# Optimization experiments

Measured on AMD Instinct MI355X. Metric: run time of the kernel, lower is better.

The kernel has to match this reference:

```python
import jax, jax.numpy as jnp
import numpy as np


def _causal_conv(x, w, b, dilation):
    # x: (B, Cin, N), w: (Cout, Cin, K) -> causal: left-pad (K-1)*dilation
    pad = (w.shape[-1] - 1) * dilation
    y = jax.lax.conv_general_dilated(
        x, w, window_strides=(1,), padding=[(pad, 0)],
        rhs_dilation=(dilation,), dimension_numbers=('NCH', 'OIH', 'NCH'))
    return y + b[None, :, None]


def setup_inputs() -> dict:
    key = jax.random.key(0)
    ks = jax.random.split(key, 8)
    B, N, C, L = 8, 32768, 16, 30
    s = 0.1  # weight scale to avoid gate saturation
    return {
        'x': jax.random.normal(ks[0], (B, N), dtype=jnp.float32) * 1000.0,  # int16-like samples
        'lengths': jax.random.randint(ks[1], (B,), N // 2, N),
        'w0': jax.random.normal(ks[2], (C, 1, 2), dtype=jnp.float32) * s,
        'b0': jnp.zeros((C,), jnp.float32),
        'wf': jax.random.normal(ks[3], (L - 1, C, C, 2), dtype=jnp.float32) * s,
        'bf': jnp.zeros((L - 1, C), jnp.float32),
        'wg': jax.random.normal(ks[4], (L - 1, C, C, 2), dtype=jnp.float32) * s,
        'bg': jnp.zeros((L - 1, C), jnp.float32),
        'wa': jax.random.normal(ks[5], (64, C), dtype=jnp.float32) * s,
        'ba': jnp.zeros((64,), jnp.float32),
        'wo': jax.random.normal(ks[6], (256, 64), dtype=jnp.float32) * s,
        'bo': jnp.zeros((256,), jnp.float32),
    }


def reference(x, lengths, w0, b0, wf, bf, wg, bg, wa, ba, wo, bo):
    L = wf.shape[0] + 1  # total layers (layer 0 is plain causal conv)
    xin = (x / 32768.0)[:, None, :]            # (B,1,N), int16 normalization 65536/2
    out0 = _causal_conv(xin, w0, b0, 1)        # (B,C,N)
    agg = out0                                 # skip aggregate
    h = xin + out0                             # residual input (broadcast 1->C channels)
    for i in range(1, L):                      # fixed small layer count
        d = 2 ** (i % 10)
        f = _causal_conv(h, wf[i - 1], bf[i - 1], d)
        g = _causal_conv(h, wg[i - 1], bg[i - 1], d)
        out = jnp.tanh(f) * jax.nn.sigmoid(g)  # gated activation unit
        agg = agg + out
        h = h + out
    a = jnp.einsum('oc,bcn->bon', wa, jax.nn.relu(agg)) + ba[None, :, None]  # agregate1x1
    o = jnp.einsum('oc,bcn->bon', wo, jax.nn.relu(a)) + bo[None, :, None]    # output1x1
    o = jax.nn.log_softmax(o, axis=1)
    mask = (jnp.arange(o.shape[-1]) < lengths[:, None]).astype(o.dtype)      # (B,N)
    return o * mask[:, None, :]
```

## Files before the change

kernel.cpp:

```cpp
#include <hip/hip_runtime.h>

#define NSEQ 32768
#define NB 8
#define NC 16
#define LBLK 1024
#define LPX (LBLK / 8)

__device__ __forceinline__ float sigm_f(float x) {
    return __fdividef(1.f, 1.f + __expf(-x));
}
__device__ __forceinline__ float tanh_f(float x) {
    return __fdividef(2.f, 1.f + __expf(-2.f * x)) - 1.f;
}

__device__ __forceinline__ int swz_bid() {
    int bid = blockIdx.x;
    return (bid & 7) * LPX + (bid >> 3);
}

__global__ __launch_bounds__(256) void k_layer0(
    const float* __restrict__ x, const float* __restrict__ w0,
    const float* __restrict__ b0, float* __restrict__ h)
{
    int tid = swz_bid() * 256 + threadIdx.x;
    int n = tid & (NSEQ - 1);
    const float inv = 1.f / 32768.f;
    float xc = x[tid] * inv;
    float xp = (n >= 1) ? x[tid - 1] * inv : 0.f;
    float v[NC];
#pragma unroll
    for (int c = 0; c < NC; c++) {
        float o = w0[c * 2] * xp + w0[c * 2 + 1] * xc + b0[c];
        v[c] = xc + o;
    }
    float4* ph = (float4*)(h + (size_t)tid * NC);
#pragma unroll
    for (int i = 0; i < 4; i++)
        ph[i] = make_float4(v[i * 4], v[i * 4 + 1], v[i * 4 + 2], v[i * 4 + 3]);
}

__global__ __launch_bounds__(256) void k_layer(
    const float* __restrict__ hin, float* __restrict__ hout,
    const float* __restrict__ wf, const float* __restrict__ bf,
    const float* __restrict__ wg, const float* __restrict__ bg, int d)
{
    int tid = swz_bid() * 256 + threadIdx.x;
    int n = tid & (NSEQ - 1);

    float hc[NC], hp[NC];
    {
        const float4* pc = (const float4*)(hin + (size_t)tid * NC);
#pragma unroll
        for (int i = 0; i < 4; i++) {
            float4 t = pc[i];
            hc[i * 4] = t.x; hc[i * 4 + 1] = t.y; hc[i * 4 + 2] = t.z; hc[i * 4 + 3] = t.w;
        }
    }
    if (n >= d) {
        const float4* pp = (const float4*)(hin + (size_t)(tid - d) * NC);
#pragma unroll
        for (int i = 0; i < 4; i++) {
            float4 t = pp[i];
            hp[i * 4] = t.x; hp[i * 4 + 1] = t.y; hp[i * 4 + 2] = t.z; hp[i * 4 + 3] = t.w;
        }
    } else {
#pragma unroll
        for (int i = 0; i < NC; i++) hp[i] = 0.f;
    }

    float f[NC], g[NC];
#pragma unroll
    for (int co = 0; co < NC; co++) { f[co] = bf[co]; g[co] = bg[co]; }

#pragma unroll
    for (int ci = 0; ci < NC; ci++) {
        float xp = hp[ci], xc = hc[ci];
#pragma unroll
        for (int co = 0; co < NC; co++) {
            f[co] = fmaf(wf[(co * NC + ci) * 2 + 0], xp, f[co]);
            f[co] = fmaf(wf[(co * NC + ci) * 2 + 1], xc, f[co]);
            g[co] = fmaf(wg[(co * NC + ci) * 2 + 0], xp, g[co]);
            g[co] = fmaf(wg[(co * NC + ci) * 2 + 1], xc, g[co]);
        }
    }

    float v[NC];
#pragma unroll
    for (int co = 0; co < NC; co++) {
        float outv = tanh_f(f[co]) * sigm_f(g[co]);
        v[co] = hc[co] + outv;
    }
    float4* po = (float4*)(hout + (size_t)tid * NC);
#pragma unroll
    for (int i = 0; i < 4; i++)
        po[i] = make_float4(v[i * 4], v[i * 4 + 1], v[i * 4 + 2], v[i * 4 + 3]);
}

__global__ __launch_bounds__(512, 2) void k_final(
    const float* __restrict__ hfin, const float* __restrict__ x,
    const int* __restrict__ lengths,
    const float* __restrict__ wa, const float* __restrict__ ba,
    const float* __restrict__ wo, const float* __restrict__ bo,
    float* __restrict__ out)
{
    __shared__ float s_r[64][17];
    __shared__ float s_ra[64][65];
    __shared__ float s_red[2][8][64];

    int t = threadIdx.x;
    int p = t & 63;
    int q = __builtin_amdgcn_readfirstlane(t >> 6);
    int blk = blockIdx.x;
    int b = blk >> 9;
    int n0 = (blk & 511) << 6;
    int n = n0 + p;
    size_t pos = (size_t)b * NSEQ + n;
    float xin = x[pos] * (1.f / 32768.f);

    if (q < 4) {
        const float4* ph = (const float4*)(hfin + pos * NC);
        float4 v = ph[q];
        s_r[p][q * 4 + 0] = fmaxf(v.x - xin, 0.f);
        s_r[p][q * 4 + 1] = fmaxf(v.y - xin, 0.f);
        s_r[p][q * 4 + 2] = fmaxf(v.z - xin, 0.f);
        s_r[p][q * 4 + 3] = fmaxf(v.w - xin, 0.f);
    }
    __syncthreads();

    {
        float r[NC];
#pragma unroll
        for (int c = 0; c < NC; c++) r[c] = s_r[p][c];
#pragma unroll
        for (int jj = 0; jj < 8; jj++) {
            int j = q * 8 + jj;
            float acc = ba[j];
#pragma unroll
            for (int c = 0; c < NC; c++) acc = fmaf(wa[j * NC + c], r[c], acc);
            s_ra[p][j] = fmaxf(acc, 0.f);
        }
    }
    __syncthreads();

    float ra[64];
#pragma unroll
    for (int j = 0; j < 64; j++) ra[j] = s_ra[p][j];

    float o[32];
    float m = -1e30f;
#pragma unroll 4
    for (int kk = 0; kk < 32; kk++) {
        int k = q * 32 + kk;
        float acc = bo[k];
#pragma unroll
        for (int j = 0; j < 64; j++) acc = fmaf(wo[k * 64 + j], ra[j], acc);
        o[kk] = acc;
        m = fmaxf(m, acc);
    }
    s_red[0][q][p] = m;
    __syncthreads();
    m = fmaxf(fmaxf(fmaxf(s_red[0][0][p], s_red[0][1][p]),
                    fmaxf(s_red[0][2][p], s_red[0][3][p])),
              fmaxf(fmaxf(s_red[0][4][p], s_red[0][5][p]),
                    fmaxf(s_red[0][6][p], s_red[0][7][p])));
    float s = 0.f;
#pragma unroll
    for (int kk = 0; kk < 32; kk++) s += __expf(o[kk] - m);
    s_red[1][q][p] = s;
    __syncthreads();
    s = ((s_red[1][0][p] + s_red[1][1][p]) + (s_red[1][2][p] + s_red[1][3][p]))
      + ((s_red[1][4][p] + s_red[1][5][p]) + (s_red[1][6][p] + s_red[1][7][p]));
    float lse = m + __logf(s);

    bool valid = n < lengths[b];
    float* po = out + ((size_t)b * 256 + q * 32) * NSEQ + n;
#pragma unroll
    for (int kk = 0; kk < 32; kk++) {
        float v = valid ? (o[kk] - lse) : 0.f;
        __builtin_nontemporal_store(v, &po[(size_t)kk * NSEQ]);
    }
}

extern "C" void kernel_launch(void* const* d_in, const int* in_sizes, int n_in,
                              void* d_out, int out_size, void* d_ws, size_t ws_size,
                              hipStream_t stream) {
    const float* x   = (const float*)d_in[0];
    const int* lens  = (const int*)d_in[1];
    const float* w0  = (const float*)d_in[2];
    const float* b0  = (const float*)d_in[3];
    const float* wf  = (const float*)d_in[4];
    const float* bf  = (const float*)d_in[5];
    const float* wg  = (const float*)d_in[6];
    const float* bg  = (const float*)d_in[7];
    const float* wa  = (const float*)d_in[8];
    const float* ba  = (const float*)d_in[9];
    const float* wo  = (const float*)d_in[10];
    const float* bo  = (const float*)d_in[11];
    float* out = (float*)d_out;

    float* hA = (float*)d_ws;
    float* hB = hA + (size_t)NB * NSEQ * NC;

    const int total = NB * NSEQ;
    dim3 blk(256);
    dim3 grd(total / 256);

    k_layer0<<<grd, blk, 0, stream>>>(x, w0, b0, hA);

    float* cur = hA;
    float* nxt = hB;
    for (int i = 1; i <= 29; i++) {
        int d = 1 << (i % 10);
        k_layer<<<grd, blk, 0, stream>>>(cur, nxt,
                                         wf + (size_t)(i - 1) * NC * NC * 2,
                                         bf + (size_t)(i - 1) * NC,
                                         wg + (size_t)(i - 1) * NC * NC * 2,
                                         bg + (size_t)(i - 1) * NC, d);
        float* tmp = cur; cur = nxt; nxt = tmp;
    }

    dim3 fgrd(NB * (NSEQ / 64));
    k_final<<<fgrd, dim3(512), 0, stream>>>(cur, x, lens, wa, ba, wo, bo, out);
}
```

Measured before the change: 670.0 us.

## Split layer kernel output channels across four waves per position

```diff
diff --git a/kernel.cpp b/kernel.cpp
--- a/kernel.cpp
+++ b/kernel.cpp
@@ -5,24 +5,22 @@
 #define NC 16
 #define LBLK 1024
 #define LPX (LBLK / 8)
+#define QGRD 4096
+#define QPX (QGRD / 8)
 
 __device__ __forceinline__ float sigm_f(float x) {
     return __fdividef(1.f, 1.f + __expf(-x));
 }
 __device__ __forceinline__ float tanh_f(float x) {
     return __fdividef(2.f, 1.f + __expf(-2.f * x)) - 1.f;
-}
-
-__device__ __forceinline__ int swz_bid() {
-    int bid = blockIdx.x;
-    return (bid & 7) * LPX + (bid >> 3);
 }
 
 __global__ __launch_bounds__(256) void k_layer0(
     const float* __restrict__ x, const float* __restrict__ w0,
     const float* __restrict__ b0, float* __restrict__ h)
 {
-    int tid = swz_bid() * 256 + threadIdx.x;
+    int bid = blockIdx.x;
+    int tid = ((bid & 7) * LPX + (bid >> 3)) * 256 + threadIdx.x;
     int n = tid & (NSEQ - 1);
     const float inv = 1.f / 32768.f;
     float xc = x[tid] * inv;
@@ -44,56 +42,60 @@
     const float* __restrict__ wf, const float* __restrict__ bf,
     const float* __restrict__ wg, const float* __restrict__ bg, int d)
 {
-    int tid = swz_bid() * 256 + threadIdx.x;
-    int n = tid & (NSEQ - 1);
+    int bid = blockIdx.x;
+    int lbid = (bid & 7) * QPX + (bid >> 3);
+    int t = threadIdx.x;
+    int pos = lbid * 64 + (t & 63);
+    int q = __builtin_amdgcn_readfirstlane(t >> 6);
+    int n = pos & (NSEQ - 1);
 
     float hc[NC], hp[NC];
     {
-        const float4* pc = (const float4*)(hin + (size_t)tid * NC);
+        const float4* pc = (const float4*)(hin + (size_t)pos * NC);
 #pragma unroll
         for (int i = 0; i < 4; i++) {
-            float4 t = pc[i];
-            hc[i * 4] = t.x; hc[i * 4 + 1] = t.y; hc[i * 4 + 2] = t.z; hc[i * 4 + 3] = t.w;
+            float4 tv = pc[i];
+            hc[i * 4] = tv.x; hc[i * 4 + 1] = tv.y; hc[i * 4 + 2] = tv.z; hc[i * 4 + 3] = tv.w;
         }
     }
     if (n >= d) {
-        const float4* pp = (const float4*)(hin + (size_t)(tid - d) * NC);
+        const float4* pp = (const float4*)(hin + (size_t)(pos - d) * NC);
 #pragma unroll
         for (int i = 0; i < 4; i++) {
-            float4 t = pp[i];
-            hp[i * 4] = t.x; hp[i * 4 + 1] = t.y; hp[i * 4 + 2] = t.z; hp[i * 4 + 3] = t.w;
+            float4 tv = pp[i];
+            hp[i * 4] = tv.x; hp[i * 4 + 1] = tv.y; hp[i * 4 + 2] = tv.z; hp[i * 4 + 3] = tv.w;
         }
     } else {
 #pragma unroll
         for (int i = 0; i < NC; i++) hp[i] = 0.f;
     }
 
-    float f[NC], g[NC];
-#pragma unroll
-    for (int co = 0; co < NC; co++) { f[co] = bf[co]; g[co] = bg[co]; }
+    const int c0 = q * 4;
+    float f[4], g[4];
+#pragma unroll
+    for (int j = 0; j < 4; j++) { f[j] = bf[c0 + j]; g[j] = bg[c0 + j]; }
 
 #pragma unroll
     for (int ci = 0; ci < NC; ci++) {
         float xp = hp[ci], xc = hc[ci];
 #pragma unroll
-        for (int co = 0; co < NC; co++) {
-            f[co] = fmaf(wf[(co * NC + ci) * 2 + 0], xp, f[co]);
-            f[co] = fmaf(wf[(co * NC + ci) * 2 + 1], xc, f[co]);
-            g[co] = fmaf(wg[(co * NC + ci) * 2 + 0], xp, g[co]);
-            g[co] = fmaf(wg[(co * NC + ci) * 2 + 1], xc, g[co]);
-        }
-    }
-
-    float v[NC];
-#pragma unroll
-    for (int co = 0; co < NC; co++) {
-        float outv = tanh_f(f[co]) * sigm_f(g[co]);
-        v[co] = hc[co] + outv;
-    }
-    float4* po = (float4*)(hout + (size_t)tid * NC);
-#pragma unroll
-    for (int i = 0; i < 4; i++)
-        po[i] = make_float4(v[i * 4], v[i * 4 + 1], v[i * 4 + 2], v[i * 4 + 3]);
+        for (int j = 0; j < 4; j++) {
+            int co = c0 + j;
+            f[j] = fmaf(wf[(co * NC + ci) * 2 + 0], xp, f[j]);
+            f[j] = fmaf(wf[(co * NC + ci) * 2 + 1], xc, f[j]);
+            g[j] = fmaf(wg[(co * NC + ci) * 2 + 0], xp, g[j]);
+            g[j] = fmaf(wg[(co * NC + ci) * 2 + 1], xc, g[j]);
+        }
+    }
+
+    float v[4];
+#pragma unroll
+    for (int j = 0; j < 4; j++) {
+        float outv = tanh_f(f[j]) * sigm_f(g[j]);
+        v[j] = hc[c0 + j] + outv;
+    }
+    float4* po = (float4*)(hout + (size_t)pos * NC + c0);
+    po[0] = make_float4(v[0], v[1], v[2], v[3]);
 }
 
 __global__ __launch_bounds__(512, 2) void k_final(
@@ -201,17 +203,13 @@
     float* hA = (float*)d_ws;
     float* hB = hA + (size_t)NB * NSEQ * NC;
 
-    const int total = NB * NSEQ;
-    dim3 blk(256);
-    dim3 grd(total / 256);
-
-    k_layer0<<<grd, blk, 0, stream>>>(x, w0, b0, hA);
+    k_layer0<<<dim3(LBLK), dim3(256), 0, stream>>>(x, w0, b0, hA);
 
     float* cur = hA;
     float* nxt = hB;
     for (int i = 1; i <= 29; i++) {
         int d = 1 << (i % 10);
-        k_layer<<<grd, blk, 0, stream>>>(cur, nxt,
+        k_layer<<<dim3(QGRD), dim3(256), 0, stream>>>(cur, nxt,
                                          wf + (size_t)(i - 1) * NC * NC * 2,
                                          bf + (size_t)(i - 1) * NC,
                                          wg + (size_t)(i - 1) * NC * NC * 2,
```

Result: faster. 638.5 us (-4.7%).
